# Kernel tuning notes

Hardware: AMD Instinct MI355X
Metric: run time of the kernel (lower is better)

Reference implementation:

```python
import jax, jax.numpy as jnp
import numpy as np

N_NODES = 100000
N_EDGES = 1600000
IN_DIM = 128
HEADS = 4
OUT_DIM = 32
NEG_SLOPE = 0.2  # DGL GATConv default


def setup_inputs() -> dict:
    key = jax.random.key(0)
    ks = jax.random.split(key, 7)
    x = jax.random.normal(ks[0], (N_NODES, IN_DIM), dtype=jnp.float32)
    edge_src = jax.random.randint(ks[1], (N_EDGES,), 0, N_NODES, dtype=jnp.int32)
    edge_dst = jax.random.randint(ks[2], (N_EDGES,), 0, N_NODES, dtype=jnp.int32)
    # Xavier-ish init for the projection / attention params
    fc_w = jax.random.normal(ks[3], (IN_DIM, HEADS * OUT_DIM), dtype=jnp.float32) / np.sqrt(IN_DIM)
    attn_l = jax.random.normal(ks[4], (HEADS, OUT_DIM), dtype=jnp.float32) / np.sqrt(OUT_DIM)
    attn_r = jax.random.normal(ks[5], (HEADS, OUT_DIM), dtype=jnp.float32) / np.sqrt(OUT_DIM)
    bias = jnp.zeros((HEADS * OUT_DIM,), dtype=jnp.float32)
    return {"x": x, "edge_src": edge_src, "edge_dst": edge_dst,
            "fc_w": fc_w, "attn_l": attn_l, "attn_r": attn_r, "bias": bias}


def reference(x, edge_src, edge_dst, fc_w, attn_l, attn_r, bias):
    N = x.shape[0]
    H, D = attn_l.shape
    # Linear projection, per-head features [N, H, D]
    feat = (x @ fc_w).reshape(N, H, D)
    # Per-node attention logits [N, H]
    el = jnp.einsum('nhd,hd->nh', feat, attn_l)
    er = jnp.einsum('nhd,hd->nh', feat, attn_r)
    # Per-edge scores e_{u->v} = leaky_relu(el[u] + er[v])  [E, H]
    e = jax.nn.leaky_relu(el[edge_src] + er[edge_dst], NEG_SLOPE)
    # Edge softmax segmented over destination node (stable via segment max)
    m = jax.ops.segment_max(e, edge_dst, num_segments=N)  # [N, H]
    m = jnp.where(jnp.isfinite(m), m, jnp.float32(0))      # zero in-degree nodes
    ex = jnp.exp(e - jax.lax.stop_gradient(m)[edge_dst])
    s = jax.ops.segment_sum(ex, edge_dst, num_segments=N)  # [N, H]
    alpha = ex / jnp.maximum(s[edge_dst], jnp.float32(1e-16))  # [E, H]
    # Weighted neighbor aggregation  out[v] = sum_u alpha * feat[u]
    msg = alpha[:, :, None] * feat[edge_src]               # [E, H, D]
    out = jax.ops.segment_sum(msg, edge_dst, num_segments=N)  # [N, H, D]
    out = out + bias.reshape(1, H, D)
    # Head mean as in the wrapper's .mean(dim=1)
    return out.mean(axis=1)  # [N, D]
```

## Files before the change

kernel.cpp:

```cpp
#include <hip/hip_runtime.h>

#define IN_DIM 128
#define HEADS 4
#define OUT_DIM 32
#define NEG 0.2f

#define NPB 256
#define NB_MAX 400
#define EPB 8192

typedef unsigned int uint;
typedef unsigned short ushort_t;
typedef short short8 __attribute__((ext_vector_type(8)));
typedef float f32x4 __attribute__((ext_vector_type(4)));
typedef uint u32x4 __attribute__((ext_vector_type(4)));

__device__ __forceinline__ uint bf16r(float f) {
    uint u = __float_as_uint(f);
    return (u + 0x7fffu + ((u >> 16) & 1u)) >> 16;
}

__global__ __launch_bounds__(256) void wt_prep_kernel(
    const float* __restrict__ fc_w, ushort_t* __restrict__ wt)
{
    int t = blockIdx.x * 256 + threadIdx.x;
    int n = t >> 7, k = t & 127;
    wt[t] = (ushort_t)bf16r(fc_w[k * 128 + n]);
}

__global__ __launch_bounds__(256) void proj_kernel(
    const float* __restrict__ x, const ushort_t* __restrict__ wt,
    const float* __restrict__ attn_l, const float* __restrict__ attn_r,
    ushort_t* __restrict__ feat16, float* __restrict__ el, float* __restrict__ er,
    int N)
{
    const int lane = threadIdx.x & 63;
    const int w    = threadIdx.x >> 6;
    const int rowbase = blockIdx.x * 64 + w * 16;
    const int c = lane & 15;
    const int g = lane >> 4;

    f32x4 acc[8];
    #pragma unroll
    for (int nt = 0; nt < 8; ++nt) acc[nt] = (f32x4){0.f, 0.f, 0.f, 0.f};

    const int arow  = rowbase + c;
    const int arowc = (arow < N) ? arow : (N - 1);
    const float* xrow = x + (size_t)arowc * 128 + g * 8;

    #pragma unroll
    for (int kk = 0; kk < 4; ++kk) {
        const float* xp = xrow + kk * 32;
        float4 f0 = *(const float4*)xp;
        float4 f1 = *(const float4*)(xp + 4);
        u32x4 au;
        au.x = bf16r(f0.x) | (bf16r(f0.y) << 16);
        au.y = bf16r(f0.z) | (bf16r(f0.w) << 16);
        au.z = bf16r(f1.x) | (bf16r(f1.y) << 16);
        au.w = bf16r(f1.z) | (bf16r(f1.w) << 16);
        short8 afrag = __builtin_bit_cast(short8, au);
        #pragma unroll
        for (int nt = 0; nt < 8; ++nt) {
            const ushort_t* wp = wt + ((nt * 16 + c) * 128 + kk * 32 + g * 8);
            u32x4 bu = *(const u32x4*)wp;
            short8 bfrag = __builtin_bit_cast(short8, bu);
            acc[nt] = __builtin_amdgcn_mfma_f32_16x16x32_bf16(afrag, bfrag, acc[nt], 0, 0, 0);
        }
    }

    float alv[4][2], arv[4][2];
    #pragma unroll
    for (int h = 0; h < 4; ++h) {
        alv[h][0] = attn_l[h * 32 + c];
        alv[h][1] = attn_l[h * 32 + 16 + c];
        arv[h][0] = attn_r[h * 32 + c];
        arv[h][1] = attn_r[h * 32 + 16 + c];
    }

    #pragma unroll
    for (int r = 0; r < 4; ++r) {
        const int node = rowbase + g * 4 + r;
        const bool ok = (node < N);
        ushort_t* fp = feat16 + (size_t)node * 128 + c;
        #pragma unroll
        for (int nt = 0; nt < 8; ++nt) {
            if (ok) fp[nt * 16] = (ushort_t)bf16r(acc[nt][r]);
        }
        #pragma unroll
        for (int h = 0; h < 4; ++h) {
            float accl = acc[2*h][r] * alv[h][0] + acc[2*h+1][r] * alv[h][1];
            float accr = acc[2*h][r] * arv[h][0] + acc[2*h+1][r] * arv[h][1];
            accl += __shfl_xor(accl, 1); accl += __shfl_xor(accl, 2);
            accl += __shfl_xor(accl, 4); accl += __shfl_xor(accl, 8);
            accr += __shfl_xor(accr, 1); accr += __shfl_xor(accr, 2);
            accr += __shfl_xor(accr, 4); accr += __shfl_xor(accr, 8);
            if (ok && c == 0) {
                el[node * 4 + h] = accl;
                er[node * 4 + h] = accr;
            }
        }
    }
}

__global__ __launch_bounds__(256) void coarse_hist_kernel(
    const int* __restrict__ edst, int* __restrict__ bucketCount, int E, int NB)
{
    __shared__ int h[NB_MAX];
    for (int t = threadIdx.x; t < NB_MAX; t += 256) h[t] = 0;
    __syncthreads();
    const int base = blockIdx.x * EPB;
    #pragma unroll
    for (int rep = 0; rep < EPB / 1024; ++rep) {
        int i = base + (rep * 256 + threadIdx.x) * 4;
        if (i + 3 < E) {
            int4 d = *(const int4*)(edst + i);
            atomicAdd(&h[d.x >> 8], 1);
            atomicAdd(&h[d.y >> 8], 1);
            atomicAdd(&h[d.z >> 8], 1);
            atomicAdd(&h[d.w >> 8], 1);
        } else {
            for (int k = 0; k < 4; ++k)
                if (i + k < E) atomicAdd(&h[edst[i + k] >> 8], 1);
        }
    }
    __syncthreads();
    for (int t = threadIdx.x; t < NB; t += 256)
        if (h[t]) atomicAdd(&bucketCount[t], h[t]);
}

__global__ __launch_bounds__(512) void bucket_scan_kernel(
    const int* __restrict__ bucketCount, int* __restrict__ bucketStart,
    int* __restrict__ bucketCursor, int* __restrict__ row_start, int NB, int N)
{
    __shared__ int p[512];
    const int t = threadIdx.x;
    int v = (t < NB) ? bucketCount[t] : 0;
    p[t] = v;
    __syncthreads();
    for (int off = 1; off < 512; off <<= 1) {
        int u = (t >= off) ? p[t - off] : 0;
        __syncthreads();
        p[t] += u;
        __syncthreads();
    }
    if (t < NB) {
        bucketStart[t]  = p[t] - v;
        bucketCursor[t] = p[t] - v;
    }
    if (t == NB - 1) {
        bucketStart[NB] = p[t];
        row_start[N]    = p[t];
    }
}

__global__ __launch_bounds__(256) void bin_kernel(
    const int* __restrict__ esrc, const int* __restrict__ edst,
    int* __restrict__ bucketCursor, uint* __restrict__ binned, int E, int NB)
{
    __shared__ int dstS[EPB];
    __shared__ int hist[NB_MAX];
    __shared__ int cur[NB_MAX];
    const int t = threadIdx.x;
    for (int k = t; k < NB_MAX; k += 256) hist[k] = 0;
    __syncthreads();

    const int base = blockIdx.x * EPB;
    #pragma unroll
    for (int rep = 0; rep < EPB / 1024; ++rep) {
        int idx4 = (rep * 256 + t) * 4;
        int i = base + idx4;
        if (i + 3 < E) {
            int4 d = *(const int4*)(edst + i);
            dstS[idx4]     = d.x; atomicAdd(&hist[d.x >> 8], 1);
            dstS[idx4 + 1] = d.y; atomicAdd(&hist[d.y >> 8], 1);
            dstS[idx4 + 2] = d.z; atomicAdd(&hist[d.z >> 8], 1);
            dstS[idx4 + 3] = d.w; atomicAdd(&hist[d.w >> 8], 1);
        } else {
            for (int k = 0; k < 4; ++k)
                if (i + k < E) {
                    int dv = edst[i + k];
                    dstS[idx4 + k] = dv;
                    atomicAdd(&hist[dv >> 8], 1);
                }
        }
    }
    __syncthreads();
    for (int k = t; k < NB; k += 256) {
        int hh = hist[k];
        cur[k] = hh ? atomicAdd(&bucketCursor[k], hh) : 0;
    }
    __syncthreads();
    const int nloc = min(EPB, E - base);
    for (int rep = 0; rep < EPB / 256; ++rep) {
        int idx = rep * 256 + t;
        if (idx < nloc) {
            int dv = dstS[idx];
            int pos = atomicAdd(&cur[dv >> 8], 1);
            int src = esrc[base + idx];
            binned[pos] = (uint)src | ((uint)(dv & 255) << 24);
        }
    }
}

__global__ __launch_bounds__(256) void fine_csr_kernel(
    const uint* __restrict__ binned, const int* __restrict__ bucketStart,
    int* __restrict__ row_start, int* __restrict__ csr, int N)
{
    __shared__ int hist[256], sc[256], cur[256];
    const int b = blockIdx.x;
    const int t = threadIdx.x;
    const int s = bucketStart[b];
    const int e = bucketStart[b + 1];

    hist[t] = 0;
    __syncthreads();
    for (int i = s + t; i < e; i += 256)
        atomicAdd(&hist[binned[i] >> 24], 1);
    __syncthreads();
    sc[t] = hist[t];
    __syncthreads();
    for (int off = 1; off < 256; off <<= 1) {
        int u = (t >= off) ? sc[t - off] : 0;
        __syncthreads();
        sc[t] += u;
        __syncthreads();
    }
    const int excl = s + sc[t] - hist[t];
    const int gn = b * NPB + t;
    if (gn < N) row_start[gn] = excl;
    cur[t] = excl;
    __syncthreads();
    for (int i = s + t; i < e; i += 256) {
        uint v = binned[i];
        int pos = atomicAdd(&cur[v >> 24], 1);
        csr[pos] = (int)(v & 0xFFFFFFu);
    }
}

__global__ __launch_bounds__(256) void aggregate_kernel(
    const uint* __restrict__ feat_b, const float* __restrict__ el,
    const float* __restrict__ er, const int* __restrict__ row_start,
    const int* __restrict__ csr, const float* __restrict__ bias,
    float* __restrict__ out, int N)
{
    int node = blockIdx.x * 4 + (threadIdx.x >> 6);
    node = __builtin_amdgcn_readfirstlane(node);
    if (node >= N) return;
    const int lane = threadIdx.x & 63;
    const int h = lane >> 4;

    const float er_vh = er[node * 4 + h];
    const int start = row_start[node];
    const int end   = row_start[node + 1];

    float a0 = 0.f, a1 = 0.f, sa = 0.f;
    float b0 = 0.f, b1 = 0.f, sb = 0.f;
    float c0 = 0.f, c1 = 0.f, sc = 0.f;
    float d0 = 0.f, d1 = 0.f, sd = 0.f;

    int idx = start;
    for (; idx + 4 <= end; idx += 4) {
        int u0 = csr[idx + 0];
        int u1 = csr[idx + 1];
        int u2 = csr[idx + 2];
        int u3 = csr[idx + 3];
        float e0 = el[u0 * 4 + h];
        float e1 = el[u1 * 4 + h];
        float e2 = el[u2 * 4 + h];
        float e3 = el[u3 * 4 + h];
        uint p0 = feat_b[(size_t)u0 * 64 + lane];
        uint p1 = feat_b[(size_t)u1 * 64 + lane];
        uint p2 = feat_b[(size_t)u2 * 64 + lane];
        uint p3 = feat_b[(size_t)u3 * 64 + lane];

        e0 += er_vh; e0 = fmaxf(e0, NEG * e0); float x0 = __expf(e0);
        e1 += er_vh; e1 = fmaxf(e1, NEG * e1); float x1 = __expf(e1);
        e2 += er_vh; e2 = fmaxf(e2, NEG * e2); float x2 = __expf(e2);
        e3 += er_vh; e3 = fmaxf(e3, NEG * e3); float x3 = __expf(e3);

        a0 = fmaf(x0, __uint_as_float(p0 << 16), a0);
        a1 = fmaf(x0, __uint_as_float(p0 & 0xffff0000u), a1);
        sa += x0;
        b0 = fmaf(x1, __uint_as_float(p1 << 16), b0);
        b1 = fmaf(x1, __uint_as_float(p1 & 0xffff0000u), b1);
        sb += x1;
        c0 = fmaf(x2, __uint_as_float(p2 << 16), c0);
        c1 = fmaf(x2, __uint_as_float(p2 & 0xffff0000u), c1);
        sc += x2;
        d0 = fmaf(x3, __uint_as_float(p3 << 16), d0);
        d1 = fmaf(x3, __uint_as_float(p3 & 0xffff0000u), d1);
        sd += x3;
    }
    for (; idx < end; ++idx) {
        int u = csr[idx];
        float e = el[u * 4 + h] + er_vh;
        e = fmaxf(e, NEG * e);
        float ex = __expf(e);
        uint p = feat_b[(size_t)u * 64 + lane];
        a0 = fmaf(ex, __uint_as_float(p << 16), a0);
        a1 = fmaf(ex, __uint_as_float(p & 0xffff0000u), a1);
        sa += ex;
    }

    float s = (sa + sb) + (sc + sd);
    s = fmaxf(s, 1e-16f);
    float r0 = ((a0 + b0) + (c0 + d0)) / s;
    float r1 = ((a1 + b1) + (c1 + d1)) / s;
    r0 += __shfl_xor(r0, 16); r0 += __shfl_xor(r0, 32);
    r1 += __shfl_xor(r1, 16); r1 += __shfl_xor(r1, 32);

    if (lane < 16) {
        int dd = lane * 2;
        float bm0 = 0.25f * (bias[dd]     + bias[32 + dd] + bias[64 + dd] + bias[96 + dd]);
        float bm1 = 0.25f * (bias[dd + 1] + bias[33 + dd] + bias[65 + dd] + bias[97 + dd]);
        float2 o;
        o.x = 0.25f * r0 + bm0;
        o.y = 0.25f * r1 + bm1;
        ((float2*)out)[(size_t)node * 16 + lane] = o;
    }
}

extern "C" void kernel_launch(void* const* d_in, const int* in_sizes, int n_in,
                              void* d_out, int out_size, void* d_ws, size_t ws_size,
                              hipStream_t stream)
{
    const float* x      = (const float*)d_in[0];
    const int*   esrc   = (const int*)  d_in[1];
    const int*   edst   = (const int*)  d_in[2];
    const float* fc_w   = (const float*)d_in[3];
    const float* attn_l = (const float*)d_in[4];
    const float* attn_r = (const float*)d_in[5];
    const float* bias   = (const float*)d_in[6];
    float* out = (float*)d_out;

    const int N = in_sizes[0] / IN_DIM;
    const int E = in_sizes[1];
    const int NB = (N + NPB - 1) / NPB;

    size_t o = 0;
    char* base = (char*)d_ws;
    auto alloc = [&](size_t bytes) -> void* {
        void* p = base + o;
        o += (bytes + 255) & ~(size_t)255;
        return p;
    };
    ushort_t* feat16   = (ushort_t*)alloc((size_t)N * 128 * sizeof(ushort_t));
    float* el          = (float*)alloc((size_t)N * 4 * sizeof(float));
    float* er          = (float*)alloc((size_t)N * 4 * sizeof(float));
    int*   row_start   = (int*)  alloc(((size_t)N + 1) * sizeof(int));
    int*   csr         = (int*)  alloc((size_t)E * sizeof(int));
    uint*  binned      = (uint*) alloc((size_t)E * sizeof(uint));
    int*   bucketCount = (int*)  alloc(NB_MAX * sizeof(int));
    int*   bucketStart = (int*)  alloc((NB_MAX + 1) * sizeof(int));
    int*   bucketCursor= (int*)  alloc(NB_MAX * sizeof(int));
    ushort_t* wt       = (ushort_t*)alloc((size_t)128 * 128 * sizeof(ushort_t));
    (void)ws_size;

    const int nblkE = (E + EPB - 1) / EPB;

    hipMemsetAsync(bucketCount, 0, NB_MAX * sizeof(int), stream);

    wt_prep_kernel<<<64, 256, 0, stream>>>(fc_w, wt);
    proj_kernel<<<(N + 63) / 64, 256, 0, stream>>>(x, wt, attn_l, attn_r,
                                                   feat16, el, er, N);
    coarse_hist_kernel<<<nblkE, 256, 0, stream>>>(edst, bucketCount, E, NB);
    bucket_scan_kernel<<<1, 512, 0, stream>>>(bucketCount, bucketStart,
                                              bucketCursor, row_start, NB, N);
    bin_kernel<<<nblkE, 256, 0, stream>>>(esrc, edst, bucketCursor, binned, E, NB);
    fine_csr_kernel<<<NB, 256, 0, stream>>>(binned, bucketStart, row_start, csr, N);
    aggregate_kernel<<<(N + 3) / 4, 256, 0, stream>>>((const uint*)feat16, el, er,
                                                      row_start, csr, bias, out, N);
}
```

Baseline: 168.6 us.

## Batch 16 edges per wave: parallel exp across lanes, then readlane-driven feature gathers

The aggregation loop now loads up to 16 neighbor indices at once, one per lane within each head group, and computes their attention exponentials in parallel. It then broadcasts each source index with readlane to issue up to 16 independent feature gathers, and applies the weights via shuffles. This removes redundant per-lane el loads and exp work and raises memory-level parallelism. The cost is extra shuffles and a larger register buffer. The edge-binning block size EPB is also reduced from 8192 to 2048, which changes the preprocessing grid granularity.

```diff
diff --git a/kernel.cpp b/kernel.cpp
--- a/kernel.cpp
+++ b/kernel.cpp
@@ -7,7 +7,7 @@
 
 #define NPB 256
 #define NB_MAX 400
-#define EPB 8192
+#define EPB 2048
 
 typedef unsigned int uint;
 typedef unsigned short ushort_t;
@@ -247,65 +247,47 @@
     node = __builtin_amdgcn_readfirstlane(node);
     if (node >= N) return;
     const int lane = threadIdx.x & 63;
-    const int h = lane >> 4;
+    const int h   = lane >> 4;
+    const int eix = lane & 15;
 
     const float er_vh = er[node * 4 + h];
     const int start = row_start[node];
     const int end   = row_start[node + 1];
 
-    float a0 = 0.f, a1 = 0.f, sa = 0.f;
-    float b0 = 0.f, b1 = 0.f, sb = 0.f;
-    float c0 = 0.f, c1 = 0.f, sc = 0.f;
-    float d0 = 0.f, d1 = 0.f, sd = 0.f;
-
-    int idx = start;
-    for (; idx + 4 <= end; idx += 4) {
-        int u0 = csr[idx + 0];
-        int u1 = csr[idx + 1];
-        int u2 = csr[idx + 2];
-        int u3 = csr[idx + 3];
-        float e0 = el[u0 * 4 + h];
-        float e1 = el[u1 * 4 + h];
-        float e2 = el[u2 * 4 + h];
-        float e3 = el[u3 * 4 + h];
-        uint p0 = feat_b[(size_t)u0 * 64 + lane];
-        uint p1 = feat_b[(size_t)u1 * 64 + lane];
-        uint p2 = feat_b[(size_t)u2 * 64 + lane];
-        uint p3 = feat_b[(size_t)u3 * 64 + lane];
-
-        e0 += er_vh; e0 = fmaxf(e0, NEG * e0); float x0 = __expf(e0);
-        e1 += er_vh; e1 = fmaxf(e1, NEG * e1); float x1 = __expf(e1);
-        e2 += er_vh; e2 = fmaxf(e2, NEG * e2); float x2 = __expf(e2);
-        e3 += er_vh; e3 = fmaxf(e3, NEG * e3); float x3 = __expf(e3);
-
-        a0 = fmaf(x0, __uint_as_float(p0 << 16), a0);
-        a1 = fmaf(x0, __uint_as_float(p0 & 0xffff0000u), a1);
-        sa += x0;
-        b0 = fmaf(x1, __uint_as_float(p1 << 16), b0);
-        b1 = fmaf(x1, __uint_as_float(p1 & 0xffff0000u), b1);
-        sb += x1;
-        c0 = fmaf(x2, __uint_as_float(p2 << 16), c0);
-        c1 = fmaf(x2, __uint_as_float(p2 & 0xffff0000u), c1);
-        sc += x2;
-        d0 = fmaf(x3, __uint_as_float(p3 << 16), d0);
-        d1 = fmaf(x3, __uint_as_float(p3 & 0xffff0000u), d1);
-        sd += x3;
-    }
-    for (; idx < end; ++idx) {
-        int u = csr[idx];
+    float r0 = 0.f, r1 = 0.f, s = 0.f;
+
+    for (int i0 = start; i0 < end; i0 += 16) {
+        const int rem = end - i0;
+        int u = csr[i0 + ((eix < rem) ? eix : (rem - 1))];
         float e = el[u * 4 + h] + er_vh;
         e = fmaxf(e, NEG * e);
-        float ex = __expf(e);
-        uint p = feat_b[(size_t)u * 64 + lane];
-        a0 = fmaf(ex, __uint_as_float(p << 16), a0);
-        a1 = fmaf(ex, __uint_as_float(p & 0xffff0000u), a1);
-        sa += ex;
-    }
-
-    float s = (sa + sb) + (sc + sd);
+        float xw = __expf(e);
+        xw = (eix < rem) ? xw : 0.f;
+        s += xw;
+
+        const int nk = (rem < 16) ? rem : 16;
+        uint pbuf[16];
+        #pragma unroll
+        for (int e2 = 0; e2 < 16; ++e2) {
+            if (e2 >= nk) break;
+            int ue = __builtin_amdgcn_readlane(u, e2);
+            pbuf[e2] = feat_b[(size_t)ue * 64 + lane];
+        }
+        #pragma unroll
+        for (int e2 = 0; e2 < 16; ++e2) {
+            if (e2 >= nk) break;
+            float xe = __shfl(xw, (lane & 48) | e2);
+            uint p = pbuf[e2];
+            r0 = fmaf(xe, __uint_as_float(p << 16), r0);
+            r1 = fmaf(xe, __uint_as_float(p & 0xffff0000u), r1);
+        }
+    }
+
+    s += __shfl_xor(s, 1); s += __shfl_xor(s, 2);
+    s += __shfl_xor(s, 4); s += __shfl_xor(s, 8);
     s = fmaxf(s, 1e-16f);
-    float r0 = ((a0 + b0) + (c0 + d0)) / s;
-    float r1 = ((a1 + b1) + (c1 + d1)) / s;
+    r0 /= s;
+    r1 /= s;
     r0 += __shfl_xor(r0, 16); r0 += __shfl_xor(r0, 32);
     r1 += __shfl_xor(r1, 16); r1 += __shfl_xor(r1, 32);
 
```

Result: slower. 240.1 us (+42.4%).
